# Kernel optimization log

Hardware: AMD Instinct MI355X
Metric: run time of the kernel (lower is better)

The kernel has to match this reference:

```python
import jax, jax.numpy as jnp
import numpy as np

N, E = 50000, 400000
C_IN, C_OUT = 64, 32
K = 9  # kernel_size 3x3


def _quad_basis(t):
    # open B-spline basis, degree 2, per torch_spline_conv: k_mod in {0,1,2}
    # t = frac(pseudo * (kernel_size - degree)) = pseudo here (kernel_size=3, degree=2)
    return jnp.stack([0.5 * (1.0 - t) ** 2, -t * t + t + 0.5, 0.5 * t * t], axis=-1)  # [E,3]


def spline_basis(pseudo):
    # kernel_size=[3,3], degree=2, open spline: v = p*(3-2)=p, floor(v)=0 for p in [0,1),
    # so weight index for combination s is exactly s = k_mod0 + 3*k_mod1.
    q0 = _quad_basis(pseudo[:, 0])  # [E,3] varies with s%3
    q1 = _quad_basis(pseudo[:, 1])  # [E,3] varies with s//3
    return (q1[:, :, None] * q0[:, None, :]).reshape(-1, K)  # [E,9]


def spline_conv(x, src, dst, B, W, root, bias, n_nodes):
    xj = x[src]  # gather source node features [E,Cin]
    msg = jnp.zeros((xj.shape[0], W.shape[-1]), x.dtype)
    for k in range(K):  # fixed small kernel loop; avoids [E,K,Cin] blowup
        msg = msg + (xj * B[:, k, None]) @ W[k]
    agg = jax.ops.segment_sum(msg, dst, num_segments=n_nodes)  # aggr='add'
    return agg + x @ root + bias


def setup_inputs() -> dict:
    key = jax.random.key(0)
    ks = jax.random.split(key, 10)
    x = jax.random.normal(ks[0], (N, C_IN), jnp.float32)
    edge_index = jax.random.randint(ks[1], (2, E), 0, N, jnp.int64)
    pseudo = jax.random.uniform(ks[2], (E, 2), jnp.float32)
    skip = jax.random.normal(ks[3], (N, C_OUT), jnp.float32)
    s1 = 1.0 / np.sqrt(C_IN)
    s2 = 1.0 / np.sqrt(C_OUT)
    W1 = jax.random.normal(ks[4], (K, C_IN, C_OUT), jnp.float32) * s1
    root1 = jax.random.normal(ks[5], (C_IN, C_OUT), jnp.float32) * s1
    b1 = jnp.zeros((C_OUT,), jnp.float32)
    W2 = jax.random.normal(ks[6], (K, C_OUT, C_OUT), jnp.float32) * s2
    root2 = jax.random.normal(ks[7], (C_OUT, C_OUT), jnp.float32) * s2
    b2 = jnp.zeros((C_OUT,), jnp.float32)
    return {"x": x, "edge_index": edge_index, "pseudo": pseudo, "skip": skip,
            "W1": W1, "root1": root1, "b1": b1, "W2": W2, "root2": root2, "b2": b2}


def reference(x, edge_index, pseudo, skip, W1, root1, b1, W2, root2, b2):
    src, dst = edge_index[0], edge_index[1]  # flow: source_to_target
    B = spline_basis(pseudo)  # [E,9]
    n = x.shape[0]
    h = jax.nn.relu(spline_conv(x, src, dst, B, W1, root1, b1, n))
    h = jnp.concatenate([h, skip], axis=1)  # [N, Cout+Cskip] == [N, Cin]
    h = jax.nn.relu(spline_conv(h, src, dst, B, W1, root1, b1, n))
    h = jax.nn.relu(spline_conv(h, src, dst, B, W2, root2, b2, n))
    return h
```

## Files before the change

kernel.cpp:

```cpp
#include <hip/hip_runtime.h>
#include <hip/hip_bf16.h>


typedef __attribute__((ext_vector_type(8))) short short8;
typedef __attribute__((ext_vector_type(4))) float f32x4;

__device__ __forceinline__ float blo(unsigned u) {
    union { unsigned u; float f; } x; x.u = u << 16; return x.f;
}
__device__ __forceinline__ float bhi(unsigned u) {
    union { unsigned u; float f; } x; x.u = u & 0xffff0000u; return x.f;
}
__device__ __forceinline__ unsigned short f2bf(float f) {
    union { float f; unsigned u; } x; x.f = f;
    unsigned r = x.u + 0x7fffu + ((x.u >> 16) & 1u);
    return (unsigned short)(r >> 16);
}
__device__ __forceinline__ short8 cvt8(const float* p) {
    float4 a = *(const float4*)p;
    float4 b = *(const float4*)(p + 4);
    short8 r;
    r[0] = (short)f2bf(a.x); r[1] = (short)f2bf(a.y);
    r[2] = (short)f2bf(a.z); r[3] = (short)f2bf(a.w);
    r[4] = (short)f2bf(b.x); r[5] = (short)f2bf(b.y);
    r[6] = (short)f2bf(b.z); r[7] = (short)f2bf(b.w);
    return r;
}

#define YROW 296

template<int MODE>
__global__ __launch_bounds__(256)
void layer_tm(const float* __restrict__ Xa, const float* __restrict__ Xb,
              const unsigned short* __restrict__ Wt,
              const float* __restrict__ bias,
              const int* __restrict__ sstart,
              const float4* __restrict__ erec,
              float* __restrict__ agg, uint4* __restrict__ msg4, int N, int E)
{
    const int CIN = (MODE == 2) ? 32 : 64;
    __shared__ __align__(16) unsigned short sY[64 * YROW];

    const int t    = threadIdx.x;
    const int wv   = t >> 6;
    const int lane = t & 63;
    const int lc   = lane & 15;
    const int q    = lane >> 4;
    const int n0   = blockIdx.x * 64;
    const int base = n0 + wv * 16;

    int na = base + lc;
    if (na >= N) na = N - 1;
    short8 a0, a1;
    if (MODE == 0) {
        const float* p = Xa + (size_t)na * 64 + q * 8;
        a0 = cvt8(p);
        a1 = cvt8(p + 32);
    } else if (MODE == 1) {
        a0 = cvt8(Xa + (size_t)na * 32 + q * 8);
        a1 = cvt8(Xb + (size_t)na * 32 + q * 8);
    } else {
        a0 = cvt8(Xa + (size_t)na * 32 + q * 8);
    }

    f32x4 acc[20];
    #pragma unroll
    for (int nt = 0; nt < 20; ++nt) acc[nt] = (f32x4){0.f, 0.f, 0.f, 0.f};

    #pragma unroll
    for (int nt = 0; nt < 20; ++nt) {
        const unsigned short* wp = Wt + ((size_t)(nt * 16 + lc)) * CIN + q * 8;
        acc[nt] = __builtin_amdgcn_mfma_f32_16x16x32_bf16(a0, *(const short8*)wp, acc[nt], 0, 0, 0);
        if (MODE != 2)
            acc[nt] = __builtin_amdgcn_mfma_f32_16x16x32_bf16(a1, *(const short8*)(wp + 32), acc[nt], 0, 0, 0);
    }

    #pragma unroll
    for (int nt = 0; nt < 18; ++nt) {
        #pragma unroll
        for (int r = 0; r < 4; ++r) {
            int nl = wv * 16 + q * 4 + r;
            sY[nl * YROW + nt * 16 + lc] = f2bf(acc[nt][r]);
        }
    }
    #pragma unroll
    for (int nt = 18; nt < 20; ++nt) {
        int c = (nt - 18) * 16 + lc;
        #pragma unroll
        for (int r = 0; r < 4; ++r) {
            int n = base + q * 4 + r;
            if (n < N) agg[(size_t)n * 32 + c] = acc[nt][r] + bias[c];
        }
    }
    __syncthreads();

    const int e0 = sstart[n0];
    const int e1 = (n0 + 64 < N) ? sstart[n0 + 64] : E;
    const int l  = t & 3;

    for (int e = e0 + (t >> 2); e < e1; e += 64) {
        const float4 r = erec[e];
        const int srcl = __float_as_int(r.x) - n0;
        const int dp   = __float_as_int(r.y);
        const float p0 = r.z, p1 = r.w;

        const float qb[3] = {0.5f * (1.f - p0) * (1.f - p0), -p0 * p0 + p0 + 0.5f, 0.5f * p0 * p0};
        const float qa[3] = {0.5f * (1.f - p1) * (1.f - p1), -p1 * p1 + p1 + 0.5f, 0.5f * p1 * p1};

        const uint4* yb = (const uint4*)(sY + srcl * YROW) + l;
        float s[8] = {0.f, 0.f, 0.f, 0.f, 0.f, 0.f, 0.f, 0.f};
        #pragma unroll
        for (int a = 0; a < 3; ++a) {
            float z[8] = {0.f, 0.f, 0.f, 0.f, 0.f, 0.f, 0.f, 0.f};
            #pragma unroll
            for (int b = 0; b < 3; ++b) {
                uint4 v = yb[(a * 3 + b) * 4];
                const float cw = qb[b];
                z[0] = fmaf(cw, blo(v.x), z[0]); z[1] = fmaf(cw, bhi(v.x), z[1]);
                z[2] = fmaf(cw, blo(v.y), z[2]); z[3] = fmaf(cw, bhi(v.y), z[3]);
                z[4] = fmaf(cw, blo(v.z), z[4]); z[5] = fmaf(cw, bhi(v.z), z[5]);
                z[6] = fmaf(cw, blo(v.w), z[6]); z[7] = fmaf(cw, bhi(v.w), z[7]);
            }
            #pragma unroll
            for (int j = 0; j < 8; ++j) s[j] = fmaf(qa[a], z[j], s[j]);
        }

        union { uint4 u; __hip_bfloat162 h[4]; } o;
        #pragma unroll
        for (int j = 0; j < 4; ++j)
            o.h[j] = __float22bfloat162_rn(float2{s[2 * j], s[2 * j + 1]});
        msg4[(size_t)dp * 4 + l] = o.u;
    }
}

__global__ __launch_bounds__(256)
void gather_kernel(const int* __restrict__ dstart,
                   const uint4* __restrict__ msg4,
                   float* __restrict__ agg, int N, int E)
{
    const int t = threadIdx.x;
    const int n = blockIdx.x * 64 + (t >> 2);
    if (n >= N) return;
    const int l = t & 3;

    const int e0 = dstart[n] - E;
    const int e1 = ((n + 1 < N) ? dstart[n + 1] : 2 * E) - E;

    float4* ap = (float4*)(agg + (size_t)n * 32 + l * 8);
    float4 A = ap[0], B = ap[1];
    const uint4* mp = msg4 + l;
    for (int e = e0; e < e1; ++e) {
        uint4 v = mp[(size_t)e * 4];
        A.x += blo(v.x); A.y += bhi(v.x); A.z += blo(v.y); A.w += bhi(v.y);
        B.x += blo(v.z); B.y += bhi(v.z); B.z += blo(v.w); B.w += bhi(v.w);
    }
    A.x = fmaxf(A.x, 0.f); A.y = fmaxf(A.y, 0.f); A.z = fmaxf(A.z, 0.f); A.w = fmaxf(A.w, 0.f);
    B.x = fmaxf(B.x, 0.f); B.y = fmaxf(B.y, 0.f); B.z = fmaxf(B.z, 0.f); B.w = fmaxf(B.w, 0.f);
    ap[0] = A; ap[1] = B;
}


__global__ __launch_bounds__(256)
void init_kernel(int* __restrict__ hist, int n2,
                 const float* __restrict__ W1, const float* __restrict__ root1,
                 const float* __restrict__ W2, const float* __restrict__ root2,
                 unsigned short* __restrict__ Wt1, unsigned short* __restrict__ Wt2)
{
    int i = blockIdx.x * 256 + threadIdx.x;
    if (i < n2) { hist[i] = 0; return; }
    int j = i - n2;
    if (j < 320 * 64) {
        int col = j / 64, k = j % 64;
        float v = (col < 288) ? W1[((size_t)(col >> 5) * 64 + k) * 32 + (col & 31)]
                              : root1[(size_t)k * 32 + (col - 288)];
        Wt1[j] = f2bf(v);
    } else if (j < 320 * 96) {
        int jj = j - 320 * 64;
        int col = jj / 32, k = jj % 32;
        float v = (col < 288) ? W2[((size_t)(col >> 5) * 32 + k) * 32 + (col & 31)]
                              : root2[(size_t)k * 32 + (col - 288)];
        Wt2[jj] = f2bf(v);
    }
}

__global__ __launch_bounds__(256)
void count_rank_kernel(const int* __restrict__ ei, int* __restrict__ hist,
                       uint2* __restrict__ rank, int N, int E)
{
    int e = blockIdx.x * 256 + threadIdx.x;
    if (e >= E) return;
    unsigned rs = atomicAdd(&hist[ei[e]], 1);
    unsigned rd = atomicAdd(&hist[N + ei[E + e]], 1);
    rank[e] = uint2{rs, rd};
}

__global__ __launch_bounds__(1024)
void scan1_kernel(int* __restrict__ hist, int* __restrict__ bsum, int n)
{
    __shared__ int s[1024];
    int tid = threadIdx.x;
    int i = blockIdx.x * 1024 + tid;
    int v = (i < n) ? hist[i] : 0;
    s[tid] = v;
    __syncthreads();
    for (int off = 1; off < 1024; off <<= 1) {
        int add = (tid >= off) ? s[tid - off] : 0;
        __syncthreads();
        s[tid] += add;
        __syncthreads();
    }
    if (i < n) hist[i] = s[tid] - v;
    if (tid == 1023) bsum[blockIdx.x] = s[1023];
}

__global__ __launch_bounds__(1024)
void scan3_kernel(int* __restrict__ hist, const int* __restrict__ bsum, int n)
{
    __shared__ int sred[128];
    int tid = threadIdx.x;
    int b = blockIdx.x;
    if (tid < 128) sred[tid] = (tid < b) ? bsum[tid] : 0;
    __syncthreads();
    for (int off = 64; off > 0; off >>= 1) {
        if (tid < off) sred[tid] += sred[tid + off];
        __syncthreads();
    }
    int pre = sred[0];
    int i = b * 1024 + tid;
    if (i < n) hist[i] += pre;
}

__global__ __launch_bounds__(256)
void scatter_plain_kernel(const int* __restrict__ ei, const float* __restrict__ pseudo,
                          const int* __restrict__ start, const uint2* __restrict__ rank,
                          float4* __restrict__ erec, int N, int E)
{
    int e = blockIdx.x * 256 + threadIdx.x;
    if (e >= E) return;
    int sv = ei[e];
    int dv = ei[E + e];
    uint2 rk = rank[e];
    int ps = start[sv] + (int)rk.x;
    int pd = start[N + dv] + (int)rk.y - E;
    float4 r;
    r.x = __int_as_float(sv);
    r.y = __int_as_float(pd);
    r.z = pseudo[2 * (size_t)e];
    r.w = pseudo[2 * (size_t)e + 1];
    erec[ps] = r;
}

extern "C" void kernel_launch(void* const* d_in, const int* in_sizes, int n_in,
                              void* d_out, int out_size, void* d_ws, size_t ws_size,
                              hipStream_t stream) {
    const float* x      = (const float*)d_in[0];
    const int*   ei     = (const int*)  d_in[1];
    const float* pseudo = (const float*)d_in[2];
    const float* skip   = (const float*)d_in[3];
    const float* W1     = (const float*)d_in[4];
    const float* root1  = (const float*)d_in[5];
    const float* b1     = (const float*)d_in[6];
    const float* W2     = (const float*)d_in[7];
    const float* root2  = (const float*)d_in[8];
    const float* b2     = (const float*)d_in[9];

    const int N = in_sizes[0] / 64;
    const int E = in_sizes[1] / 2;
    float* out = (float*)d_out;

    unsigned short* msg = (unsigned short*)d_ws;
    float*  agg1  = (float*)(msg + (size_t)E * 32);
    float4* erec  = (float4*)(agg1 + (size_t)N * 32);
    uint2*  rank  = (uint2*)(erec + E);
    int*    start = (int*)(rank + E);
    int*    bsum  = start + 2 * N;
    unsigned short* Wt1 = (unsigned short*)(bsum + 256);
    unsigned short* Wt2 = Wt1 + 320 * 64;

    const dim3 blk(256);
    const int tb   = (N + 63) / 64;
    const int gb   = (N + 63) / 64;
    const int e256 = (E + 255) / 256;
    const int n2k  = (2 * N + 1023) / 1024;
    const int itot = 2 * N + 320 * 96;
    int* dstart = start + N;

    init_kernel<<<(itot + 255) / 256, blk, 0, stream>>>(start, 2 * N, W1, root1, W2, root2, Wt1, Wt2);
    count_rank_kernel<<<e256, blk, 0, stream>>>(ei, start, rank, N, E);
    scan1_kernel<<<n2k, 1024, 0, stream>>>(start, bsum, 2 * N);
    scan3_kernel<<<n2k, 1024, 0, stream>>>(start, bsum, 2 * N);
    scatter_plain_kernel<<<e256, blk, 0, stream>>>(ei, pseudo, start, rank, erec, N, E);

    layer_tm<0><<<tb, blk, 0, stream>>>(x, nullptr, Wt1, b1, start, erec, agg1, (uint4*)msg, N, E);
    gather_kernel<<<gb, blk, 0, stream>>>(dstart, (const uint4*)msg, agg1, N, E);
    layer_tm<1><<<tb, blk, 0, stream>>>(agg1, skip, Wt1, b1, start, erec, agg1, (uint4*)msg, N, E);
    gather_kernel<<<gb, blk, 0, stream>>>(dstart, (const uint4*)msg, agg1, N, E);
    layer_tm<2><<<tb, blk, 0, stream>>>(agg1, nullptr, Wt2, b2, start, erec, out, (uint4*)msg, N, E);
    gather_kernel<<<gb, blk, 0, stream>>>(dstart, (const uint4*)msg, out, N, E);
}
```

Measured before the change: 265.3 us.

## Fuse per-node gather aggregation into the next layer's transform kernel

The gather (segment-sum plus ReLU) of each layer's messages now runs at the start of the next layer's transform kernel, building the MFMA A operand straight from the aggregated values instead of a separate gather kernel writing agg back to memory. Message and aggregate buffers are double-buffered (msgA/msgB, agg1/agg2) so one kernel can read the previous messages while writing new ones. This removes two kernel launches and a round trip of the [N,32] aggregate through global memory. The cost is an uneven per-lane edge loop before the MFMA phase, which can add divergence, and the rank buffer now shares storage with msgB.

```diff
diff --git a/kernel.cpp b/kernel.cpp
--- a/kernel.cpp
+++ b/kernel.cpp
@@ -29,71 +29,12 @@
 
 #define YROW 296
 
-template<int MODE>
-__global__ __launch_bounds__(256)
-void layer_tm(const float* __restrict__ Xa, const float* __restrict__ Xb,
-              const unsigned short* __restrict__ Wt,
-              const float* __restrict__ bias,
-              const int* __restrict__ sstart,
-              const float4* __restrict__ erec,
-              float* __restrict__ agg, uint4* __restrict__ msg4, int N, int E)
-{
-    const int CIN = (MODE == 2) ? 32 : 64;
-    __shared__ __align__(16) unsigned short sY[64 * YROW];
-
-    const int t    = threadIdx.x;
-    const int wv   = t >> 6;
-    const int lane = t & 63;
-    const int lc   = lane & 15;
-    const int q    = lane >> 4;
-    const int n0   = blockIdx.x * 64;
-    const int base = n0 + wv * 16;
-
-    int na = base + lc;
-    if (na >= N) na = N - 1;
-    short8 a0, a1;
-    if (MODE == 0) {
-        const float* p = Xa + (size_t)na * 64 + q * 8;
-        a0 = cvt8(p);
-        a1 = cvt8(p + 32);
-    } else if (MODE == 1) {
-        a0 = cvt8(Xa + (size_t)na * 32 + q * 8);
-        a1 = cvt8(Xb + (size_t)na * 32 + q * 8);
-    } else {
-        a0 = cvt8(Xa + (size_t)na * 32 + q * 8);
-    }
-
-    f32x4 acc[20];
-    #pragma unroll
-    for (int nt = 0; nt < 20; ++nt) acc[nt] = (f32x4){0.f, 0.f, 0.f, 0.f};
-
-    #pragma unroll
-    for (int nt = 0; nt < 20; ++nt) {
-        const unsigned short* wp = Wt + ((size_t)(nt * 16 + lc)) * CIN + q * 8;
-        acc[nt] = __builtin_amdgcn_mfma_f32_16x16x32_bf16(a0, *(const short8*)wp, acc[nt], 0, 0, 0);
-        if (MODE != 2)
-            acc[nt] = __builtin_amdgcn_mfma_f32_16x16x32_bf16(a1, *(const short8*)(wp + 32), acc[nt], 0, 0, 0);
-    }
-
-    #pragma unroll
-    for (int nt = 0; nt < 18; ++nt) {
-        #pragma unroll
-        for (int r = 0; r < 4; ++r) {
-            int nl = wv * 16 + q * 4 + r;
-            sY[nl * YROW + nt * 16 + lc] = f2bf(acc[nt][r]);
-        }
-    }
-    #pragma unroll
-    for (int nt = 18; nt < 20; ++nt) {
-        int c = (nt - 18) * 16 + lc;
-        #pragma unroll
-        for (int r = 0; r < 4; ++r) {
-            int n = base + q * 4 + r;
-            if (n < N) agg[(size_t)n * 32 + c] = acc[nt][r] + bias[c];
-        }
-    }
-    __syncthreads();
-
+__device__ __forceinline__ void m_phase(const unsigned short* sY,
+                                        const int* __restrict__ sstart,
+                                        const float4* __restrict__ erec,
+                                        uint4* __restrict__ msgOut,
+                                        int n0, int t, int N, int E)
+{
     const int e0 = sstart[n0];
     const int e1 = (n0 + 64 < N) ? sstart[n0 + 64] : E;
     const int l  = t & 3;
@@ -129,13 +70,114 @@
         #pragma unroll
         for (int j = 0; j < 4; ++j)
             o.h[j] = __float22bfloat162_rn(float2{s[2 * j], s[2 * j + 1]});
-        msg4[(size_t)dp * 4 + l] = o.u;
-    }
-}
-
-__global__ __launch_bounds__(256)
-void gather_kernel(const int* __restrict__ dstart,
-                   const uint4* __restrict__ msg4,
+        msgOut[(size_t)dp * 4 + l] = o.u;
+    }
+}
+
+template<int NHALF>
+__device__ __forceinline__ void t_core(short8 a0, short8 a1,
+                                       const unsigned short* __restrict__ Wt,
+                                       const float* __restrict__ bias,
+                                       unsigned short* sY, float* __restrict__ aggOut,
+                                       int base, int wv, int lc, int q, int N)
+{
+    const int CIN = NHALF * 32;
+    f32x4 acc[20];
+    #pragma unroll
+    for (int nt = 0; nt < 20; ++nt) acc[nt] = (f32x4){0.f, 0.f, 0.f, 0.f};
+
+    #pragma unroll
+    for (int nt = 0; nt < 20; ++nt) {
+        const unsigned short* wp = Wt + ((size_t)(nt * 16 + lc)) * CIN + q * 8;
+        acc[nt] = __builtin_amdgcn_mfma_f32_16x16x32_bf16(a0, *(const short8*)wp, acc[nt], 0, 0, 0);
+        if (NHALF == 2)
+            acc[nt] = __builtin_amdgcn_mfma_f32_16x16x32_bf16(a1, *(const short8*)(wp + 32), acc[nt], 0, 0, 0);
+    }
+
+    #pragma unroll
+    for (int nt = 0; nt < 18; ++nt) {
+        #pragma unroll
+        for (int r = 0; r < 4; ++r) {
+            int nl = wv * 16 + q * 4 + r;
+            sY[nl * YROW + nt * 16 + lc] = f2bf(acc[nt][r]);
+        }
+    }
+    #pragma unroll
+    for (int nt = 18; nt < 20; ++nt) {
+        int c = (nt - 18) * 16 + lc;
+        #pragma unroll
+        for (int r = 0; r < 4; ++r) {
+            int n = base + q * 4 + r;
+            if (n < N) aggOut[(size_t)n * 32 + c] = acc[nt][r] + bias[c];
+        }
+    }
+}
+
+__global__ __launch_bounds__(256)
+void layer_tm0(const float* __restrict__ Xa,
+               const unsigned short* __restrict__ Wt, const float* __restrict__ bias,
+               const int* __restrict__ sstart, const float4* __restrict__ erec,
+               float* __restrict__ aggOut, uint4* __restrict__ msgOut, int N, int E)
+{
+    __shared__ __align__(16) unsigned short sY[64 * YROW];
+    const int t = threadIdx.x, wv = t >> 6, lane = t & 63;
+    const int lc = lane & 15, q = lane >> 4;
+    const int n0 = blockIdx.x * 64, base = n0 + wv * 16;
+
+    int na = base + lc;
+    if (na >= N) na = N - 1;
+    const float* p = Xa + (size_t)na * 64 + q * 8;
+    short8 a0 = cvt8(p);
+    short8 a1 = cvt8(p + 32);
+
+    t_core<2>(a0, a1, Wt, bias, sY, aggOut, base, wv, lc, q, N);
+    __syncthreads();
+    m_phase(sY, sstart, erec, msgOut, n0, t, N, E);
+}
+
+template<int MODE>
+__global__ __launch_bounds__(256)
+void layer_gtm(const float* __restrict__ aggPrev, const float* __restrict__ skipv,
+               const unsigned short* __restrict__ Wt, const float* __restrict__ bias,
+               const int* __restrict__ sstart, const int* __restrict__ dstart,
+               const float4* __restrict__ erec,
+               const uint4* __restrict__ msgIn, uint4* __restrict__ msgOut,
+               float* __restrict__ aggOut, int N, int E)
+{
+    __shared__ __align__(16) unsigned short sY[64 * YROW];
+    const int t = threadIdx.x, wv = t >> 6, lane = t & 63;
+    const int lc = lane & 15, q = lane >> 4;
+    const int n0 = blockIdx.x * 64, base = n0 + wv * 16;
+
+    int na = base + lc;
+    if (na >= N) na = N - 1;
+
+    const float* ap = aggPrev + (size_t)na * 32 + q * 8;
+    float4 r0 = *(const float4*)ap;
+    float4 r1 = *(const float4*)(ap + 4);
+    float h[8] = {r0.x, r0.y, r0.z, r0.w, r1.x, r1.y, r1.z, r1.w};
+    const int ge0 = dstart[na] - E;
+    const int ge1 = ((na + 1 < N) ? dstart[na + 1] : 2 * E) - E;
+    for (int e = ge0; e < ge1; ++e) {
+        uint4 v = msgIn[(size_t)e * 4 + q];
+        h[0] += blo(v.x); h[1] += bhi(v.x); h[2] += blo(v.y); h[3] += bhi(v.y);
+        h[4] += blo(v.z); h[5] += bhi(v.z); h[6] += blo(v.w); h[7] += bhi(v.w);
+    }
+    union { short8 v; __hip_bfloat162 h2[4]; } pk;
+    #pragma unroll
+    for (int j = 0; j < 4; ++j)
+        pk.h2[j] = __float22bfloat162_rn(float2{fmaxf(h[2 * j], 0.f), fmaxf(h[2 * j + 1], 0.f)});
+    short8 a0 = pk.v;
+    short8 a1;
+    if (MODE == 1) a1 = cvt8(skipv + (size_t)na * 32 + q * 8);
+
+    t_core<(MODE == 1) ? 2 : 1>(a0, a1, Wt, bias, sY, aggOut, base, wv, lc, q, N);
+    __syncthreads();
+    m_phase(sY, sstart, erec, msgOut, n0, t, N, E);
+}
+
+__global__ __launch_bounds__(256)
+void gather_kernel(const int* __restrict__ dstart, const uint4* __restrict__ msg4,
                    float* __restrict__ agg, int N, int E)
 {
     const int t = threadIdx.x;
@@ -268,14 +310,16 @@
     const int E = in_sizes[1] / 2;
     float* out = (float*)d_out;
 
-    unsigned short* msg = (unsigned short*)d_ws;
-    float*  agg1  = (float*)(msg + (size_t)E * 32);
-    float4* erec  = (float4*)(agg1 + (size_t)N * 32);
-    uint2*  rank  = (uint2*)(erec + E);
-    int*    start = (int*)(rank + E);
+    unsigned short* msgA = (unsigned short*)d_ws;
+    unsigned short* msgB = msgA + (size_t)E * 32;
+    float*  agg1  = (float*)(msgB + (size_t)E * 32);
+    float*  agg2  = agg1 + (size_t)N * 32;
+    float4* erec  = (float4*)(agg2 + (size_t)N * 32);
+    int*    start = (int*)(erec + E);
     int*    bsum  = start + 2 * N;
     unsigned short* Wt1 = (unsigned short*)(bsum + 256);
     unsigned short* Wt2 = Wt1 + 320 * 64;
+    uint2*  rank  = (uint2*)msgB;
 
     const dim3 blk(256);
     const int tb   = (N + 63) / 64;
@@ -291,10 +335,10 @@
     scan3_kernel<<<n2k, 1024, 0, stream>>>(start, bsum, 2 * N);
     scatter_plain_kernel<<<e256, blk, 0, stream>>>(ei, pseudo, start, rank, erec, N, E);
 
-    layer_tm<0><<<tb, blk, 0, stream>>>(x, nullptr, Wt1, b1, start, erec, agg1, (uint4*)msg, N, E);
-    gather_kernel<<<gb, blk, 0, stream>>>(dstart, (const uint4*)msg, agg1, N, E);
-    layer_tm<1><<<tb, blk, 0, stream>>>(agg1, skip, Wt1, b1, start, erec, agg1, (uint4*)msg, N, E);
-    gather_kernel<<<gb, blk, 0, stream>>>(dstart, (const uint4*)msg, agg1, N, E);
-    layer_tm<2><<<tb, blk, 0, stream>>>(agg1, nullptr, Wt2, b2, start, erec, out, (uint4*)msg, N, E);
-    gather_kernel<<<gb, blk, 0, stream>>>(dstart, (const uint4*)msg, out, N, E);
-}
+    layer_tm0<<<tb, blk, 0, stream>>>(x, Wt1, b1, start, erec, agg1, (uint4*)msgA, N, E);
+    layer_gtm<1><<<tb, blk, 0, stream>>>(agg1, skip, Wt1, b1, start, dstart, erec,
+                                         (const uint4*)msgA, (uint4*)msgB, agg2, N, E);
+    layer_gtm<2><<<tb, blk, 0, stream>>>(agg2, nullptr, Wt2, b2, start, dstart, erec,
+                                         (const uint4*)msgB, (uint4*)msgA, out, N, E);
+    gather_kernel<<<gb, blk, 0, stream>>>(dstart, (const uint4*)msgA, out, N, E);
+}
```

After: 264.1 us. About the same (-0.5%).
